# Kernel optimization log

Measured on AMD Instinct MI355X. Metric: run time of the kernel, lower is better.

Reference implementation:

```python
import jax, jax.numpy as jnp
import numpy as np

B, S, D = 2, 2048, 2048
NQ, NKV, H = 16, 8, 256
G = NQ // NKV
SOFT_CAP = 50.0
WINDOW = 1024
MAX_WAVELENGTH = 10000.0


def _rope(x, start_index=0):
    # keras_hub RotaryEmbedding (rotate-half) followed by Gemma's interleave
    # reshape: stack(split(x,2,-1),axis=-1).reshape(shape). Net effect:
    # out[..., 2i] = x1*cos - x2*sin, out[..., 2i+1] = x2*cos + x1*sin.
    b, s, n, h = x.shape
    half = h // 2
    inv_freq = 1.0 / (MAX_WAVELENGTH ** (jnp.arange(0, h, 2, dtype=jnp.float32) / h))
    positions = start_index + jnp.arange(s, dtype=jnp.float32)
    freq = positions[:, None] * inv_freq[None, :]            # (s, h/2)
    cos = jnp.cos(freq)[None, :, None, :].astype(x.dtype)     # (1,s,1,h/2)
    sin = jnp.sin(freq)[None, :, None, :].astype(x.dtype)
    x1, x2 = x[..., :half], x[..., half:]
    r1 = x1 * cos - x2 * sin
    r2 = x2 * cos + x1 * sin
    return jnp.stack([r1, r2], axis=-1).reshape(b, s, n, h)


def setup_inputs() -> dict:
    key = jax.random.key(0)
    ks = jax.random.split(key, 5)
    x = jax.random.normal(ks[0], (B, S, D), dtype=jnp.float32)
    Wq = jax.random.normal(ks[1], (NQ, D, H), dtype=jnp.float32) * 0.02
    Wk = jax.random.normal(ks[2], (NKV, D, H), dtype=jnp.float32) * 0.02
    Wv = jax.random.normal(ks[3], (NKV, D, H), dtype=jnp.float32) * 0.02
    Wo = jax.random.normal(ks[4], (NQ, H, D), dtype=jnp.float32) * 0.02
    attention_mask = jnp.tril(jnp.ones((S, S), dtype=jnp.float32))  # causal
    return {"x": x, "Wq": Wq, "Wk": Wk, "Wv": Wv, "Wo": Wo,
            "attention_mask": attention_mask}


def reference(x, Wq, Wk, Wv, Wo, attention_mask):
    q = _rope(jnp.einsum('btd,ndh->btnh', x, Wq))   # (B,S,NQ,H)
    k = _rope(jnp.einsum('bsd,kdh->bskh', x, Wk))   # (B,S,NKV,H)
    v = jnp.einsum('bsd,kdh->bskh', x, Wv)          # (B,S,NKV,H)

    q = q * jnp.asarray(1.0 / np.sqrt(H), dtype=q.dtype)
    q = q.reshape(B, S, NKV, G, H)
    logits = jnp.einsum('btkgh,bskh->bkgts', q, k).astype(jnp.float32)

    # logit soft-cap
    logits = jnp.tanh(logits / SOFT_CAP) * SOFT_CAP

    # sliding-window band AND causal mask
    ones = jnp.ones((S, S), dtype=jnp.float32)
    sliding = jnp.triu(ones, -(WINDOW - 1)) * jnp.tril(ones, WINDOW - 1)
    mask = sliding * attention_mask                  # (S,S)

    # keras Softmax with mask: masked positions get -1e9 (fp32)
    masked = jnp.where(mask[None, None, None, :, :] > 0, logits,
                       jnp.float32(-1e9))
    probs = jax.nn.softmax(masked, axis=-1).astype(x.dtype)

    av = jnp.einsum('bkgts,bskh->btkgh', probs, v).reshape(B, S, NQ, H)

    # zero rows with no attended tokens (original causal mask)
    na = jnp.all(attention_mask == 0, axis=-1, keepdims=True)[..., None]  # (S,1,1)
    av = jnp.where(na, jnp.zeros_like(av), av)

    return jnp.einsum('btnh,nhd->btd', av, Wo)
```

## Files before the change

### kernel.cpp

```cpp
#include <hip/hip_runtime.h>
#include <stdint.h>

typedef __bf16 bf16_t;
typedef __bf16 bf16x8 __attribute__((ext_vector_type(8)));
typedef __bf16 bf16x4 __attribute__((ext_vector_type(4)));
typedef float f32x4 __attribute__((ext_vector_type(4)));

#define DEV static __device__ __forceinline__

#define SB 2
#define SS 2048
#define SD 2048
#define SNQ 16
#define SNKV 8
#define SH 256
#define SWIN 1024
#define QKVP 8192

DEV void async_ld16(const void* g, void* lds) {
  __builtin_amdgcn_global_load_lds(
      (const __attribute__((address_space(1))) void*)g,
      (__attribute__((address_space(3))) void*)lds, 16, 0, 0);
}

__global__ __launch_bounds__(256) void prep_kernel(
    const float* __restrict__ x, const float* __restrict__ Wq,
    const float* __restrict__ Wk, const float* __restrict__ Wv,
    const float* __restrict__ Wo, bf16_t* __restrict__ xb,
    bf16_t* __restrict__ wqkvT, bf16_t* __restrict__ woT) {
  __shared__ bf16_t T[64 * 72];
  int bid = blockIdx.x;
  if (bid < 8192) {
    const int i = bid * 256 + threadIdx.x;
    float4 v = ((const float4*)x)[i];
    bf16x4 o = {(bf16_t)v.x, (bf16_t)v.y, (bf16_t)v.z, (bf16_t)v.w};
    *(bf16x4*)(xb + (size_t)i * 4) = o;
    return;
  }
  bid -= 8192;
  const float* ip;
  bf16_t* op;
  int R, C, r0, c0;
  if (bid < 4096) {
    const int zg = bid >> 7, rest = bid & 127;
    r0 = (rest >> 2) * 64;
    c0 = (rest & 3) * 64;
    ip = (zg < 16) ? (Wq + (size_t)zg * SD * SH)
       : (zg < 24) ? (Wk + (size_t)(zg - 16) * SD * SH)
                   : (Wv + (size_t)(zg - 24) * SD * SH);
    op = wqkvT + (size_t)zg * SD * SH;
    R = SD; C = SH;
  } else {
    bid -= 4096;
    r0 = (bid >> 5) * 64;
    c0 = (bid & 31) * 64;
    ip = Wo; op = woT; R = SNQ * SH; C = SD;
  }
  const int tc = threadIdx.x & 15;
  const int tr = threadIdx.x >> 4;
#pragma unroll
  for (int i = 0; i < 4; ++i) {
    const int r = tr + i * 16;
    float4 v = *(const float4*)(ip + (size_t)(r0 + r) * C + c0 + tc * 4);
    float vv[4] = {v.x, v.y, v.z, v.w};
#pragma unroll
    for (int e = 0; e < 4; ++e) {
      const int row = tc * 4 + e;
      *(bf16_t*)((char*)T + row * 144 + ((r * 2) ^ (((row >> 3) & 7) << 4))) =
          (bf16_t)vv[e];
    }
  }
  __syncthreads();
  const int tc2 = threadIdx.x & 7, tr2 = threadIdx.x >> 3;
#pragma unroll
  for (int i = 0; i < 2; ++i) {
    const int row = tr2 + i * 32;
    bf16x8 v = *(const bf16x8*)((const char*)T + row * 144 +
                                ((tc2 * 16) ^ (((row >> 3) & 7) << 4)));
    *(bf16x8*)(op + (size_t)(c0 + row) * R + r0 + tc2 * 8) = v;
  }
}

template <int BN, int MODE>
__global__ __launch_bounds__(512, 1) void gemm8p(const bf16_t* __restrict__ A,
                                                 const bf16_t* __restrict__ Bt,
                                                 void* __restrict__ Cout,
                                                 bf16_t* __restrict__ kbp,
                                                 bf16_t* __restrict__ vtp,
                                                 int M, int N, int K) {
  constexpr int WM = (BN == 256) ? 2 : 4;
  constexpr int WN = 8 / WM;
  constexpr int MQ = 4 / WM;
  constexpr int BH = BN / 128;
  constexpr int SMEM = 65536 + BH * 32768;
  __shared__ char smem[SMEM];
  bf16_t* AsBase = (bf16_t*)smem;
  bf16_t* BsBase = (bf16_t*)(smem + 65536);

  const int tid = threadIdx.x, lane = tid & 63, wid = tid >> 6;
  const int xcd = blockIdx.x & 7, ii = blockIdx.x >> 3;
  int by, bx;
  if (BN == 256) { by = (xcd & 1) * 8 + (ii >> 3); bx = (xcd >> 1) * 8 + (ii & 7); }
  else           { by = (xcd & 3) * 4 + (ii >> 3); bx = (xcd >> 2) * 8 + (ii & 7); }
  const int row0 = by << 8, col0 = bx * BN;
  const int wr = wid / WN, wc = wid % WN;
  const int lr = lane & 15, hi = lane >> 4;

  const bf16_t* Arow = A + (size_t)row0 * K;
  const bf16_t* Brow = Bt + (size_t)col0 * K;

  auto stageHA = [&](int t, int h) {
#pragma unroll
    for (int i = 0; i < 2; ++i) {
      const int f = tid + (i << 9);
      const int r = (h << 7) + (f >> 3), pc = f & 7;
      async_ld16(Arow + (size_t)r * K + (t << 6) + (pc ^ (r & 7)) * 8,
                 (char*)(AsBase + (t & 1) * (256 * 64)) + (h << 14) + f * 16);
    }
  };
  auto stageHB = [&](int t, int h) {
#pragma unroll
    for (int i = 0; i < 2; ++i) {
      const int f = tid + (i << 9);
      const int r = (h << 7) + (f >> 3), pc = f & 7;
      async_ld16(Brow + (size_t)r * K + (t << 6) + (pc ^ (r & 7)) * 8,
                 (char*)(BsBase + (t & 1) * (BN * 64)) + (h << 14) + f * 16);
    }
  };

  f32x4 acc[4 * MQ][4];
#pragma unroll
  for (int m = 0; m < 4 * MQ; ++m)
#pragma unroll
    for (int n = 0; n < 4; ++n) acc[m][n] = f32x4{0.f, 0.f, 0.f, 0.f};

  const int NT = K >> 6;
  if (BH == 2) {
    stageHB(0, 0); stageHA(0, 0); stageHB(0, 1); stageHA(0, 1);
    asm volatile("s_waitcnt vmcnt(4)" ::: "memory");
  } else {
    stageHB(0, 0); stageHA(0, 0); stageHA(0, 1);
    asm volatile("s_waitcnt vmcnt(2)" ::: "memory");
  }
  __builtin_amdgcn_s_barrier();
  __builtin_amdgcn_sched_barrier(0);

  for (int t = 0; t < NT; ++t) {
    const bool pre = (t + 1 < NT);
    const char* Ab = (const char*)(AsBase + (t & 1) * (256 * 64));
    const char* Bb = (const char*)(BsBase + (t & 1) * (BN * 64));

#pragma unroll
    for (int pa = 0; pa < 2; ++pa) {
      bf16x8 af[2][MQ][2];
#pragma unroll
      for (int qq = 0; qq < 2; ++qq)
#pragma unroll
        for (int mq = 0; mq < MQ; ++mq)
#pragma unroll
          for (int ks = 0; ks < 2; ++ks) {
            const int r = (pa * 2 + qq) * 64 + mq * (16 * WM) + wr * 16 + lr;
            af[qq][mq][ks] = *(const bf16x8*)(Ab + r * 128 +
                                              ((((ks << 2) + hi) ^ (r & 7)) << 4));
          }
#pragma unroll
      for (int pb = 0; pb < 2; ++pb) {
        bf16x8 bfr[2][2];
#pragma unroll
        for (int bn = 0; bn < 2; ++bn)
#pragma unroll
          for (int ks = 0; ks < 2; ++ks) {
            const int r = (pb * 2 + bn) * (16 * WN) + wc * 16 + lr;
            bfr[bn][ks] = *(const bf16x8*)(Bb + r * 128 +
                                           ((((ks << 2) + hi) ^ (r & 7)) << 4));
          }
        if (pre) {
          if (pa == 0 && pb == 0) stageHB(t + 1, 0);
          if (pa == 0 && pb == 1) stageHA(t + 1, 0);
          if (pa == 1 && pb == 0 && BH == 2) stageHB(t + 1, 1);
          if (pa == 1 && pb == 1) stageHA(t + 1, 1);
        }
        __builtin_amdgcn_s_setprio(1);
#pragma unroll
        for (int qq = 0; qq < 2; ++qq)
#pragma unroll
          for (int mq = 0; mq < MQ; ++mq)
#pragma unroll
            for (int bn = 0; bn < 2; ++bn)
#pragma unroll
              for (int ks = 0; ks < 2; ++ks)
                acc[(pa * 2 + qq) * MQ + mq][pb * 2 + bn] =
                    __builtin_amdgcn_mfma_f32_16x16x32_bf16(
                        af[qq][mq][ks], bfr[bn][ks],
                        acc[(pa * 2 + qq) * MQ + mq][pb * 2 + bn], 0, 0, 0);
        __builtin_amdgcn_s_setprio(0);

        if (pa == 0 && pb == 0 && BH == 2) {
          if (pre) asm volatile("s_waitcnt vmcnt(4)" ::: "memory");
          else     asm volatile("s_waitcnt vmcnt(2)" ::: "memory");
          __builtin_amdgcn_s_barrier();
          __builtin_amdgcn_sched_barrier(0);
        }
        if (pa == 0 && pb == 1) {
          if (pre) asm volatile("s_waitcnt vmcnt(4)" ::: "memory");
          else     asm volatile("s_waitcnt vmcnt(0)" ::: "memory");
          __builtin_amdgcn_s_barrier();
          __builtin_amdgcn_sched_barrier(0);
        }
        if (pa == 1 && pb == 1 && pre) {
          if (BH == 2) asm volatile("s_waitcnt vmcnt(4)" ::: "memory");
          else         asm volatile("s_waitcnt vmcnt(2)" ::: "memory");
          __builtin_amdgcn_s_barrier();
          __builtin_amdgcn_sched_barrier(0);
        }
      }
    }
  }

  if (MODE == 1 && bx >= 16 && bx < 24) {
    const int kv = bx - 16;
#pragma unroll
    for (int mf = 0; mf < 4 * MQ; ++mf) {
      const int r = row0 + (mf / MQ) * 64 + (mf % MQ) * (16 * WM) + wr * 16 + hi * 4;
#pragma unroll
      for (int nfp = 0; nfp < 2; ++nfp) {
        const int h = nfp * 64 + wc * 16 + lr;
        const float inv = __expf((float)h * -0.07195578f);
#pragma unroll
        for (int j = 0; j < 4; ++j) {
          const int rg = r + j;
          const int tpos = rg & (SS - 1), b = rg >> 11;
          const float fr = (float)tpos * inv;
          const float cs = __cosf(fr), sn = __sinf(fr);
          const float x1 = acc[mf][nfp][j], x2 = acc[mf][nfp + 2][j];
          bf16_t* kp = kbp + ((size_t)(b * SNKV + kv) * SS + tpos) * SH + h;
          kp[0] = (bf16_t)(x1 * cs - x2 * sn);
          kp[128] = (bf16_t)(x2 * cs + x1 * sn);
        }
      }
    }
  } else if (MODE == 1 && bx >= 24) {
    bf16_t* T = (bf16_t*)smem;
    __syncthreads();
    const int kv = bx - 24;
#pragma unroll
    for (int mf = 0; mf < 4 * MQ; ++mf) {
      const int tl = (mf / MQ) * 64 + (mf % MQ) * (16 * WM) + wr * 16 + hi * 4;
#pragma unroll
      for (int nf = 0; nf < 4; ++nf) {
        const int h = nf * (16 * WN) + wc * 16 + lr;
        bf16x4 v4 = {(bf16_t)acc[mf][nf][0], (bf16_t)acc[mf][nf][1],
                     (bf16_t)acc[mf][nf][2], (bf16_t)acc[mf][nf][3]};
        *(bf16x4*)((char*)T + h * 512 + ((tl * 2) ^ ((h & 7) << 4))) = v4;
      }
    }
    __syncthreads();
    const int b = row0 >> 11, t0b = row0 & (SS - 1);
    bf16_t* vbase = vtp + (size_t)(b * SNKV + kv) * SH * SS;
#pragma unroll
    for (int it = 0; it < 16; ++it) {
      const int f = tid + (it << 9);
      const int h = f >> 5, sl = f & 31;
      bf16x8 v = *(const bf16x8*)((const char*)T + h * 512 +
                                  ((sl << 4) ^ ((h & 7) << 4)));
      *(bf16x8*)(vbase + (size_t)h * SS + t0b + sl * 8) = v;
    }
  } else {
#pragma unroll
    for (int mf = 0; mf < 4 * MQ; ++mf) {
      const int r = row0 + (mf / MQ) * 64 + (mf % MQ) * (16 * WM) + wr * 16 + hi * 4;
#pragma unroll
      for (int nf = 0; nf < 4; ++nf) {
        const int c = col0 + nf * (16 * WN) + wc * 16 + lr;
#pragma unroll
        for (int j = 0; j < 4; ++j) {
          if (MODE == 2)
            ((float*)Cout)[(size_t)(r + j) * N + c] = acc[mf][nf][j];
          else
            ((bf16_t*)Cout)[(size_t)(r + j) * N + c] = (bf16_t)acc[mf][nf][j];
        }
      }
    }
  }
}

#define QB 128
#define KVB 64
#define PP 72

__global__ __launch_bounds__(512, 2) void attn_kernel(
    const bf16_t* __restrict__ Q,
    const bf16_t* __restrict__ Kt,
    const bf16_t* __restrict__ Vt,
    bf16_t* __restrict__ AV) {
  __shared__ bf16_t Ks[2][KVB * SH];
  __shared__ bf16_t Vs[2][SH * KVB];
  __shared__ bf16_t Ps[QB * PP];

  const int tid = threadIdx.x, lane = tid & 63, wid = tid >> 6;
  const int x = blockIdx.x & 7;
  const int y = blockIdx.x >> 3;
  const int qt = 15 - (y & 15);
  const int head = (x << 1) | ((y >> 4) & 1);
  const int b = y >> 5;
  const int kvh = x;
  const int t0 = qt << 7;
  const int trw = t0 + wid * 16;
  const int lr = lane & 15, hi = lane >> 4;
  const int lk = hi << 3;
  const int lq = hi;

  bf16x8 qf[8];
  {
    const bf16_t* qp = Q + ((size_t)(b * SS + trw + lr)) * QKVP + head * SH + lk;
#pragma unroll
    for (int ks = 0; ks < 8; ++ks) qf[ks] = *(const bf16x8*)(qp + ks * 32);
    const float tpos = (float)(trw + lr);
#pragma unroll
    for (int ks = 0; ks < 4; ++ks) {
      bf16x8 a = qf[ks], b2 = qf[ks + 4];
      bf16x8 ra, rb;
#pragma unroll
      for (int e = 0; e < 8; ++e) {
        float c_ = (float)(ks * 32 + lk + e);
        float inv = __expf(c_ * -0.07195578f);
        float fr = tpos * inv;
        float cs = __cosf(fr), sn = __sinf(fr);
        float x1 = (float)a[e], x2 = (float)b2[e];
        ra[e] = (bf16_t)((x1 * cs - x2 * sn) * 0.0625f);
        rb[e] = (bf16_t)((x2 * cs + x1 * sn) * 0.0625f);
      }
      qf[ks] = ra; qf[ks + 4] = rb;
    }
  }

  f32x4 o[16];
#pragma unroll
  for (int i = 0; i < 16; ++i) o[i] = f32x4{0.f, 0.f, 0.f, 0.f};
  float lsum[4] = {0.f, 0.f, 0.f, 0.f};

  const bf16_t* Kb = Kt + (size_t)(b * SNKV + kvh) * SS * SH;
  const bf16_t* Vb = Vt + (size_t)(b * SNKV + kvh) * SH * SS;

  const int sv0 = (t0 >= SWIN) ? ((t0 >> 6) - 16) : 0;
  const int sv1 = (t0 >> 6) + 1;

  auto stage = [&](int s0, int d) {
#pragma unroll
    for (int it = 0; it < 4; ++it) {
      const int f = tid + (it << 9);
      {
        const int r = f >> 5, pc = f & 31;
        const int sc = pc ^ (r & 7);
        async_ld16(Kb + (size_t)(s0 + r) * SH + sc * 8, (char*)Ks[d] + f * 16);
      }
      {
        const int r = f >> 3, pc = f & 7;
        const int sc = pc ^ (r & 7);
        async_ld16(Vb + (size_t)r * SS + s0 + sc * 8, (char*)Vs[d] + f * 16);
      }
    }
  };

  stage(sv0 << 6, 0);
  __syncthreads();

  int cur = 0;
  for (int sv = sv0; sv <= sv1; ++sv, cur ^= 1) {
    if (sv < sv1) stage((sv + 1) << 6, cur ^ 1);

    const int s0 = sv << 6;
    const bool skip = (s0 > trw + 15) || (s0 + 63 < trw - (SWIN - 1));
    if (!skip) {
      const bf16_t* Kc = Ks[cur];
      const bf16_t* Vc = Vs[cur];
      f32x4 sacc[4];
#pragma unroll
      for (int nt = 0; nt < 4; ++nt) sacc[nt] = f32x4{0.f, 0.f, 0.f, 0.f};
      __builtin_amdgcn_s_setprio(1);
#pragma unroll
      for (int ks = 0; ks < 8; ++ks) {
#pragma unroll
        for (int nt = 0; nt < 4; ++nt) {
          const int R = nt * 16 + lr;
          bf16x8 kf = *(const bf16x8*)((const char*)Kc + R * 512 +
                                       (((ks * 4 + hi) ^ (R & 7)) << 4));
          sacc[nt] = __builtin_amdgcn_mfma_f32_16x16x32_bf16(qf[ks], kf, sacc[nt], 0, 0, 0);
        }
      }
      __builtin_amdgcn_s_setprio(0);

      const bool full = (s0 + 63 <= trw) && (s0 >= trw + 15 - (SWIN - 1));
      if (full) {
#pragma unroll
        for (int nt = 0; nt < 4; ++nt) {
#pragma unroll
          for (int j = 0; j < 4; ++j) {
            float u = sacc[nt][j] * 0.04f;
            float th = 50.f - 100.f * __builtin_amdgcn_rcpf(__expf(u) + 1.f);
            float p = __expf(th);
            lsum[j] += p;
            Ps[(wid * 16 + lq * 4 + j) * PP + nt * 16 + lr] = (bf16_t)p;
          }
        }
      } else {
#pragma unroll
        for (int nt = 0; nt < 4; ++nt) {
          const int s_ = s0 + nt * 16 + lr;
#pragma unroll
          for (int j = 0; j < 4; ++j) {
            const int t_ = trw + lq * 4 + j;
            float u = sacc[nt][j] * 0.04f;
            float th = 50.f - 100.f * __builtin_amdgcn_rcpf(__expf(u) + 1.f);
            const bool valid = (s_ <= t_) && (t_ - s_ < SWIN);
            float p = valid ? __expf(th) : 0.f;
            lsum[j] += p;
            Ps[(wid * 16 + lq * 4 + j) * PP + nt * 16 + lr] = (bf16_t)p;
          }
        }
      }

      __builtin_amdgcn_s_setprio(1);
#pragma unroll
      for (int ks = 0; ks < 2; ++ks) {
        bf16x8 pf = *(const bf16x8*)&Ps[(wid * 16 + lr) * PP + ks * 32 + lk];
#pragma unroll
        for (int nt = 0; nt < 16; ++nt) {
          const int R = nt * 16 + lr;
          bf16x8 vf = *(const bf16x8*)((const char*)Vc + R * 128 +
                                       (((ks * 4 + hi) ^ (R & 7)) << 4));
          o[nt] = __builtin_amdgcn_mfma_f32_16x16x32_bf16(pf, vf, o[nt], 0, 0, 0);
        }
      }
      __builtin_amdgcn_s_setprio(0);
    }

    __syncthreads();
  }

#pragma unroll
  for (int j = 0; j < 4; ++j) {
    float l = lsum[j];
    l += __shfl_xor(l, 1);
    l += __shfl_xor(l, 2);
    l += __shfl_xor(l, 4);
    l += __shfl_xor(l, 8);
    const float inv = 1.f / l;
    const int t_ = trw + lq * 4 + j;
    bf16_t* op = AV + ((size_t)(b * SS + t_)) * (SNQ * SH) + head * SH;
#pragma unroll
    for (int nt = 0; nt < 16; ++nt) op[nt * 16 + lr] = (bf16_t)(o[nt][j] * inv);
  }
}

extern "C" void kernel_launch(void* const* d_in, const int* in_sizes, int n_in,
                              void* d_out, int out_size, void* d_ws, size_t ws_size,
                              hipStream_t stream) {
  const float* x = (const float*)d_in[0];
  const float* Wq = (const float*)d_in[1];
  const float* Wk = (const float*)d_in[2];
  const float* Wv = (const float*)d_in[3];
  const float* Wo = (const float*)d_in[4];
  float* out = (float*)d_out;

  char* ws = (char*)d_ws;
  size_t off = 0;
  auto alloc = [&](size_t elems) {
    bf16_t* p = (bf16_t*)(ws + off);
    off += ((elems * 2 + 255) & ~(size_t)255);
    return p;
  };
  const size_t MS = (size_t)SB * SS;
  bf16_t* xb     = alloc(MS * SD);
  bf16_t* wqkvT  = alloc((size_t)QKVP * SD);
  bf16_t* woT    = alloc((size_t)SD * SNQ * SH);
  bf16_t* qkv    = alloc(MS * QKVP);
  bf16_t* kb     = alloc(MS * SNKV * SH);
  bf16_t* vt     = alloc(MS * SNKV * SH);
  bf16_t* av     = alloc(MS * SNQ * SH);
  (void)ws_size;

  prep_kernel<<<14336, 256, 0, stream>>>(x, Wq, Wk, Wv, Wo, xb, wqkvT, woT);

  gemm8p<256, 1><<<512, 512, 0, stream>>>(xb, wqkvT, qkv, kb, vt, 4096, QKVP, 2048);

  attn_kernel<<<512, 512, 0, stream>>>(qkv, kb, vt, av);

  gemm8p<128, 2><<<256, 512, 0, stream>>>(av, woT, out, nullptr, nullptr, 4096, 2048, 4096);
}
```

Measured before the change: 325.5 us.

## Restructure GEMM main loop to load all B fragments once per K-tile

```diff
diff --git a/kernel.cpp b/kernel.cpp
--- a/kernel.cpp
+++ b/kernel.cpp
@@ -135,13 +135,10 @@
     for (int n = 0; n < 4; ++n) acc[m][n] = f32x4{0.f, 0.f, 0.f, 0.f};
 
   const int NT = K >> 6;
-  if (BH == 2) {
-    stageHB(0, 0); stageHA(0, 0); stageHB(0, 1); stageHA(0, 1);
-    asm volatile("s_waitcnt vmcnt(4)" ::: "memory");
-  } else {
-    stageHB(0, 0); stageHA(0, 0); stageHA(0, 1);
-    asm volatile("s_waitcnt vmcnt(2)" ::: "memory");
-  }
+  stageHB(0, 0);
+  if (BH == 2) stageHB(0, 1);
+  stageHA(0, 0); stageHA(0, 1);
+  asm volatile("s_waitcnt vmcnt(2)" ::: "memory");
   __builtin_amdgcn_s_barrier();
   __builtin_amdgcn_sched_barrier(0);
 
@@ -149,70 +146,61 @@
     const bool pre = (t + 1 < NT);
     const char* Ab = (const char*)(AsBase + (t & 1) * (256 * 64));
     const char* Bb = (const char*)(BsBase + (t & 1) * (BN * 64));
-
-#pragma unroll
-    for (int pa = 0; pa < 2; ++pa) {
-      bf16x8 af[2][MQ][2];
-#pragma unroll
-      for (int qq = 0; qq < 2; ++qq)
-#pragma unroll
-        for (int mq = 0; mq < MQ; ++mq)
+    bf16x8 bfr[4][2];
+
+#pragma unroll
+    for (int q = 0; q < 4; ++q) {
+      if (q == 0) {
+#pragma unroll
+        for (int nf = 0; nf < 4; ++nf)
 #pragma unroll
           for (int ks = 0; ks < 2; ++ks) {
-            const int r = (pa * 2 + qq) * 64 + mq * (16 * WM) + wr * 16 + lr;
-            af[qq][mq][ks] = *(const bf16x8*)(Ab + r * 128 +
-                                              ((((ks << 2) + hi) ^ (r & 7)) << 4));
-          }
-#pragma unroll
-      for (int pb = 0; pb < 2; ++pb) {
-        bf16x8 bfr[2][2];
-#pragma unroll
-        for (int bn = 0; bn < 2; ++bn)
-#pragma unroll
-          for (int ks = 0; ks < 2; ++ks) {
-            const int r = (pb * 2 + bn) * (16 * WN) + wc * 16 + lr;
-            bfr[bn][ks] = *(const bf16x8*)(Bb + r * 128 +
+            const int r = nf * (16 * WN) + wc * 16 + lr;
+            bfr[nf][ks] = *(const bf16x8*)(Bb + r * 128 +
                                            ((((ks << 2) + hi) ^ (r & 7)) << 4));
           }
-        if (pre) {
-          if (pa == 0 && pb == 0) stageHB(t + 1, 0);
-          if (pa == 0 && pb == 1) stageHA(t + 1, 0);
-          if (pa == 1 && pb == 0 && BH == 2) stageHB(t + 1, 1);
-          if (pa == 1 && pb == 1) stageHA(t + 1, 1);
-        }
-        __builtin_amdgcn_s_setprio(1);
-#pragma unroll
-        for (int qq = 0; qq < 2; ++qq)
-#pragma unroll
-          for (int mq = 0; mq < MQ; ++mq)
-#pragma unroll
-            for (int bn = 0; bn < 2; ++bn)
-#pragma unroll
-              for (int ks = 0; ks < 2; ++ks)
-                acc[(pa * 2 + qq) * MQ + mq][pb * 2 + bn] =
-                    __builtin_amdgcn_mfma_f32_16x16x32_bf16(
-                        af[qq][mq][ks], bfr[bn][ks],
-                        acc[(pa * 2 + qq) * MQ + mq][pb * 2 + bn], 0, 0, 0);
-        __builtin_amdgcn_s_setprio(0);
-
-        if (pa == 0 && pb == 0 && BH == 2) {
-          if (pre) asm volatile("s_waitcnt vmcnt(4)" ::: "memory");
-          else     asm volatile("s_waitcnt vmcnt(2)" ::: "memory");
-          __builtin_amdgcn_s_barrier();
-          __builtin_amdgcn_sched_barrier(0);
-        }
-        if (pa == 0 && pb == 1) {
-          if (pre) asm volatile("s_waitcnt vmcnt(4)" ::: "memory");
-          else     asm volatile("s_waitcnt vmcnt(0)" ::: "memory");
-          __builtin_amdgcn_s_barrier();
-          __builtin_amdgcn_sched_barrier(0);
-        }
-        if (pa == 1 && pb == 1 && pre) {
-          if (BH == 2) asm volatile("s_waitcnt vmcnt(4)" ::: "memory");
-          else         asm volatile("s_waitcnt vmcnt(2)" ::: "memory");
-          __builtin_amdgcn_s_barrier();
-          __builtin_amdgcn_sched_barrier(0);
-        }
+      }
+      bf16x8 af[MQ][2];
+#pragma unroll
+      for (int mq = 0; mq < MQ; ++mq)
+#pragma unroll
+        for (int ks = 0; ks < 2; ++ks) {
+          const int r = q * 64 + mq * (16 * WM) + wr * 16 + lr;
+          af[mq][ks] = *(const bf16x8*)(Ab + r * 128 +
+                                        ((((ks << 2) + hi) ^ (r & 7)) << 4));
+        }
+      if (pre) {
+        if (BH == 2) {
+          if (q == 0) stageHB(t + 1, 0);
+          if (q == 1) stageHB(t + 1, 1);
+          if (q == 2) stageHA(t + 1, 0);
+          if (q == 3) stageHA(t + 1, 1);
+        } else {
+          if (q == 0) stageHB(t + 1, 0);
+          if (q == 1) stageHA(t + 1, 0);
+          if (q == 2) stageHA(t + 1, 1);
+        }
+      }
+      __builtin_amdgcn_s_setprio(1);
+#pragma unroll
+      for (int mq = 0; mq < MQ; ++mq)
+#pragma unroll
+        for (int nf = 0; nf < 4; ++nf)
+#pragma unroll
+          for (int ks = 0; ks < 2; ++ks)
+            acc[q * MQ + mq][nf] = __builtin_amdgcn_mfma_f32_16x16x32_bf16(
+                af[mq][ks], bfr[nf][ks], acc[q * MQ + mq][nf], 0, 0, 0);
+      __builtin_amdgcn_s_setprio(0);
+      if (q == 1) {
+        if (pre) asm volatile("s_waitcnt vmcnt(4)" ::: "memory");
+        else     asm volatile("s_waitcnt vmcnt(0)" ::: "memory");
+        __builtin_amdgcn_s_barrier();
+        __builtin_amdgcn_sched_barrier(0);
+      }
+      if (q == 3 && pre) {
+        asm volatile("s_waitcnt vmcnt(2)" ::: "memory");
+        __builtin_amdgcn_s_barrier();
+        __builtin_amdgcn_sched_barrier(0);
       }
     }
   }
```

After: 322.4 us (median of 2 runs). About the same (-1.0%).
